# Performance work log

Measured on AMD Instinct MI355X. Metric: run time of the kernel, lower is better.

The kernel has to match this reference:

```python
import jax, jax.numpy as jnp
import numpy as np

N, K, F, E = 1024, 32, 8192, 64   # nodes, max degree, input feats, embed dim
H1, H2 = 128, 64                  # fc MLP widths (layers=[128,64])
T = 3                             # fixed traversal steps per node (original: data-dependent while)


def setup_inputs() -> dict:
    key = jax.random.key(0)
    ks = jax.random.split(key, 8)
    return {
        "feature_origin": jax.random.normal(ks[0], (N, F), jnp.float32),
        "neighbors": jax.random.randint(ks[1], (N, K), 0, N),
        "W_emb": jax.random.normal(ks[2], (F, E), jnp.float32) / np.float32(np.sqrt(F)),
        "b_emb": jnp.zeros((E,), jnp.float32),
        "W1": jax.random.normal(ks[3], (2 * E, H1), jnp.float32) / np.float32(np.sqrt(2 * E)),
        "b1": jnp.zeros((H1,), jnp.float32),
        "W2": jax.random.normal(ks[4], (H1, H2), jnp.float32) / np.float32(np.sqrt(H1)),
        "b2": jnp.zeros((H2,), jnp.float32),
        "W_lk": jax.random.normal(ks[5], (H2, 1), jnp.float32) / np.float32(np.sqrt(H2)),
        "b_lk": jnp.zeros((1,), jnp.float32),
        "W_act": jax.random.normal(ks[6], (H2, 2), jnp.float32) / np.float32(np.sqrt(H2)),
        "b_act": jnp.zeros((2,), jnp.float32),
    }


def reference(feature_origin, neighbors, W_emb, b_emb, W1, b1, W2, b2, W_lk, b_lk, W_act, b_act):
    embed = lambda x: jax.nn.relu(x @ W_emb + b_emb)
    feat0 = embed(feature_origin)  # [N, E]

    def node_step(feature, i):
        idx = neighbors[i]                      # [K] neighbor node ids
        own_orig = feature_origin[i]            # [F]
        valid0 = jnp.ones((K,), bool)
        sum0 = jnp.zeros((F,), feature.dtype)   # running sum of signal-neighbor raw feats
        cnt0 = jnp.zeros((), feature.dtype)
        done0 = jnp.zeros((), bool)

        def step(carry, _):
            feature, valid, sum_hv, cnt, done = carry
            # candidate features: feature[v] if v > 0 else ending zeros (faithful to `v > 0` check)
            cand = jnp.where((idx > 0)[:, None], feature[idx], 0.0)              # [K, E]
            cand = jnp.concatenate([cand, jnp.zeros((1, E), feature.dtype)], 0)  # ending slot -> [K+1, E]
            fi = feature[i]
            s = jnp.concatenate([jnp.broadcast_to(fi, (K + 1, E)), cand], -1)    # [K+1, 2E]
            hidden = jax.nn.relu(jax.nn.relu(s @ W1 + b1) @ W2 + b2)             # [K+1, H2]
            lk = (hidden @ W_lk + b_lk)[:, 0]                                    # [K+1]
            mask = jnp.concatenate([valid, jnp.ones((1,), bool)])                # ending always selectable
            ut = jnp.argmax(jnp.where(mask, lk, -jnp.inf))                       # greedy (in lieu of Categorical)
            new_done = done | (ut == K)
            ut_c = jnp.minimum(ut, K - 1)
            at = jnp.argmax(hidden[ut_c] @ W_act + b_act)                        # greedy action
            u = idx[ut_c]
            u_orig = feature_origin[u]
            take = (at == 1).astype(feature.dtype)
            # hv = mean([signal feats] (+ origin[u] if at==1) + origin[i])
            hv_mean = (sum_hv + take * u_orig + own_orig) / (cnt + take + 1.0)
            new_fi = embed(hv_mean)
            new_fu = embed(u_orig)
            upd = jnp.logical_not(new_done)
            feature = feature.at[i].set(jnp.where(upd, new_fi, feature[i]))
            feature = feature.at[u].set(jnp.where(upd, new_fu, feature[u]))
            sum_hv = jnp.where(upd, sum_hv + take * u_orig, sum_hv)
            cnt = jnp.where(upd, cnt + take, cnt)
            valid = valid.at[ut_c].set(jnp.where(upd, False, valid[ut_c]))  # pop chosen neighbor
            return (feature, valid, sum_hv, cnt, new_done), None

        (feature, _, _, _, _), _ = jax.lax.scan(step, (feature, valid0, sum0, cnt0, done0), None, length=T)
        return feature, None

    feature, _ = jax.lax.scan(jax.checkpoint(node_step), feat0, jnp.arange(N))
    return feature
```

## Files before the change

kernel.cpp:

```cpp
#include <hip/hip_runtime.h>


typedef float f32x4 __attribute__((ext_vector_type(4)));
typedef float f32x2 __attribute__((ext_vector_type(2)));
typedef short bf16x8 __attribute__((ext_vector_type(8)));

__device__ __forceinline__ unsigned short bf16_rne(float x) {
  unsigned u = __builtin_bit_cast(unsigned, x);
  unsigned r = (u + 0x7FFFu + ((u >> 16) & 1u)) >> 16;
  return (unsigned short)r;
}
__device__ __forceinline__ float bf16_f(unsigned short h) {
  return __builtin_bit_cast(float, ((unsigned)h) << 16);
}
__device__ __forceinline__ void split3(float x, unsigned short& h, unsigned short& m,
                                       unsigned short& l) {
  h = bf16_rne(x); float r  = x - bf16_f(h);
  m = bf16_rne(r); float r2 = r - bf16_f(m);
  l = bf16_rne(r2);
}
__device__ __forceinline__ void split3_pk(float x, float y,
                                          unsigned& ph, unsigned& pm, unsigned& pl) {
  asm("v_cvt_pk_bf16_f32 %0, %1, %2" : "=v"(ph) : "v"(x), "v"(y));
  float xh = __builtin_bit_cast(float, ph << 16);
  float yh = __builtin_bit_cast(float, ph & 0xFFFF0000u);
  float rx = x - xh, ry = y - yh;
  asm("v_cvt_pk_bf16_f32 %0, %1, %2" : "=v"(pm) : "v"(rx), "v"(ry));
  float xm = __builtin_bit_cast(float, pm << 16);
  float ym = __builtin_bit_cast(float, pm & 0xFFFF0000u);
  float r2x = rx - xm, r2y = ry - ym;
  asm("v_cvt_pk_bf16_f32 %0, %1, %2" : "=v"(pl) : "v"(r2x), "v"(r2y));
}

__device__ __forceinline__ void bar_lgkm() {
  __builtin_amdgcn_sched_barrier(0);
  asm volatile("s_waitcnt lgkmcnt(0)" ::: "memory");
  __builtin_amdgcn_s_barrier();
  asm volatile("" ::: "memory");
  __builtin_amdgcn_sched_barrier(0);
}

__global__ __launch_bounds__(256) void k_embed(
    const float* __restrict__ X, const float* __restrict__ W_emb,
    const float* __restrict__ b_emb,
    float* __restrict__ G0, float* __restrict__ feat0, float* __restrict__ out)
{
  const int t = threadIdx.x;
  const int j = t & 63;
  const int node = (blockIdx.x << 2) + (t >> 6);
  const float* __restrict__ xr = X + (size_t)node * 8192;
  const float* __restrict__ wp = W_emb + j;
  double a0 = 0.0, a1 = 0.0, a2 = 0.0, a3 = 0.0;
  for (int f = 0; f < 8192; f += 4) {
    float x0 = xr[f + 0], x1 = xr[f + 1], x2 = xr[f + 2], x3 = xr[f + 3];
    a0 = fma((double)x0, (double)wp[(f + 0) << 6], a0);
    a1 = fma((double)x1, (double)wp[(f + 1) << 6], a1);
    a2 = fma((double)x2, (double)wp[(f + 2) << 6], a2);
    a3 = fma((double)x3, (double)wp[(f + 3) << 6], a3);
  }
  float g = (float)((a0 + a1) + (a2 + a3));
  const int o = node * 64 + j;
  G0[o] = g;
  float f0 = fmaxf(g + b_emb[j], 0.0f);
  feat0[o] = f0;
  out[o] = f0;
}

__global__ __launch_bounds__(128) void k_y0(
    const float* __restrict__ feat0, const float* __restrict__ W1,
    float* __restrict__ Y0, float* __restrict__ Y)
{
  const int c = threadIdx.x;
  const int i = blockIdx.x;
  const float* __restrict__ fr = feat0 + i * 64;
  float acc = 0.0f;
  #pragma unroll 8
  for (int e = 0; e < 64; ++e)
    acc = fmaf(fr[e], W1[(64 + e) * 128 + c], acc);
  Y0[i * 128 + c] = acc;
  Y[i * 128 + c] = acc;
}

__global__ __launch_bounds__(512, 2) void k_serial(
    const int* __restrict__ neighbors,
    const float* __restrict__ W1, const float* __restrict__ b1,
    const float* __restrict__ W2, const float* __restrict__ b2,
    const float* __restrict__ W_lk, const float* __restrict__ b_lk,
    const float* __restrict__ W_act, const float* __restrict__ b_act,
    const float* __restrict__ b_emb,
    const float* __restrict__ G0, const float* __restrict__ feat0,
    const float* __restrict__ Y0, float* __restrict__ Y,
    float* __restrict__ feature)
{
  __shared__ __align__(16) float W1T[128 * 130];
  __shared__ __align__(16) unsigned short Ash[48 * 128];
  __shared__ __align__(16) unsigned short Asm[48 * 128];
  __shared__ __align__(16) unsigned short Asl[48 * 128];
  __shared__ __align__(16) float Yl[32][128];
  __shared__ __align__(16) float G0l[32][64];
  __shared__ __align__(16) float a1s[128];
  __shared__ __align__(16) float fis[64];
  __shared__ __align__(16) float b1s[128];
  __shared__ __align__(16) float lkrawT[16][64];
  __shared__ __align__(16) f32x2 p01rawT[16][32];
  __shared__ __align__(16) unsigned keybuf[64];
  __shared__ int idxs[32];
  __shared__ int s_u, s_upd;
  __shared__ unsigned s_mu, s_mi;

  const int t = threadIdx.x;
  const int lane = t & 63;
  const int wave = t >> 6;
  const int l15 = lane & 15;
  const int lg = lane >> 4;
  const int mt = wave & 3;
  const int m0 = mt << 4;
  const int c16 = (mt << 2) + lg;

  unsigned* const uAsh = (unsigned*)Ash;
  unsigned* const uAsm = (unsigned*)Asm;
  unsigned* const uAsl = (unsigned*)Asl;

  for (int idx = t; idx < 16384; idx += 512) {
    int e = idx >> 7, c = idx & 127;
    W1T[c * 130 + e] = W1[e * 128 + c];
  }
  if (t < 128) b1s[t] = b1[t];
  for (int idx = 33 * 64 + t; idx < 48 * 64; idx += 512) {
    uAsh[idx] = 0u; uAsm[idx] = 0u; uAsl[idx] = 0u;
  }
  const float blkv = b_lk[0];
  const float ba0 = b_act[0];
  const float ba1 = b_act[1];
  const float bembr = b_emb[lane];
  bf16x8 wh[4], wm[4], wl[4];
  #pragma unroll
  for (int kc = 0; kc < 4; ++kc) {
    bf16x8 vh, vm, vl;
    #pragma unroll
    for (int e = 0; e < 8; ++e) {
      int k = (kc << 5) + (lg << 3) + e;
      float x = W2[k * 64 + m0 + l15];
      unsigned short sh, sm, sl;
      split3(x, sh, sm, sl);
      vh[e] = (short)sh; vm[e] = (short)sm; vl[e] = (short)sl;
    }
    wh[kc] = vh; wm[kc] = vm; wl[kc] = vl;
  }
  const f32x4 c0init = *(const f32x4*)&b2[m0 + (lg << 2)];
  const f32x4 wl4 = *(const f32x4*)&W_lk[m0 + (lg << 2)];
  f32x4 wa0v, wa1v;
  #pragma unroll
  for (int r = 0; r < 4; ++r) {
    f32x2 w2a = *(const f32x2*)&W_act[(m0 + (lg << 2) + r) << 1];
    wa0v[r] = w2a[0]; wa1v[r] = w2a[1];
  }
  int kk[4]; unsigned wb[4]; const float2* ylp[4];
  #pragma unroll
  for (int n = 0; n < 4; ++n) {
    kk[n] = wave + (n << 3);
    wb[n] = (unsigned)((kk[n] << 6) + (lane ^ ((kk[n] & 7) << 2)));
    ylp[n] = (const float2*)&Yl[kk[n]][lane << 1];
  }
  const unsigned wb32 = 2048u + (unsigned)lane;
  const int ntA = (wave < 4) ? 0 : 1;
  const int rowA = (ntA << 4) + l15;
  const int rowB = 32 + l15;
  int aoA[4], aoB[4];
  #pragma unroll
  for (int kc = 0; kc < 4; ++kc) {
    aoA[kc] = (rowA << 7) + ((((kc << 2) + lg) ^ (rowA & 7)) << 3);
    aoB[kc] = (rowB << 7) + ((((kc << 2) + lg) ^ (rowB & 7)) << 3);
  }
  const float2* const a1p = (const float2*)&a1s[lane << 1];
  unsigned vm = 0xFFFFFFFFu; float cntf = 0.f; int done = 0;
  int ridx = 0; float gisr = 0.f, sumgr = 0.f;

  for (int i = 0; i < 1024; ++i) {
    __syncthreads();
    #pragma unroll
    for (int p = 0; p < 2; ++p) {
      int fi = (p << 9) + t;
      int k = fi >> 5;
      int c4 = (fi & 31) << 2;
      int v = neighbors[(i << 5) + k];
      *(float4*)&Yl[k][c4] = *(const float4*)&Y[v * 128 + c4];
    }
    {
      int k = t >> 4;
      int c4 = (t & 15) << 2;
      int v = neighbors[(i << 5) + k];
      *(float4*)&G0l[k][c4] = *(const float4*)&G0[v * 64 + c4];
    }
    if (t < 64) fis[t] = feature[(i << 6) + t];
    if (t < 32) idxs[t] = neighbors[(i << 5) + t];
    bar_lgkm();
    if (t < 128) {
      float aa0 = b1s[t], aa1 = 0.0f;
      const float* w1r = &W1T[t * 130];
      #pragma unroll 8
      for (int e = 0; e < 64; e += 2) {
        f32x2 wv = *(const f32x2*)&w1r[e];
        aa0 = fmaf(fis[e],     wv[0], aa0);
        aa1 = fmaf(fis[e + 1], wv[1], aa1);
      }
      a1s[t] = aa0 + aa1;
    }
    int vn[4];
    #pragma unroll
    for (int n = 0; n < 4; ++n) vn[n] = idxs[kk[n]];
    if (wave == 0) {
      ridx = idxs[lane & 31];
      gisr = G0[(i << 6) + lane];
      sumgr = 0.f; vm = 0xFFFFFFFFu; cntf = 0.f; done = 0;
    }
    bar_lgkm();

    for (int st = 0; st < 3; ++st) {
      {
        float2 av = *a1p;
        #pragma unroll
        for (int n = 0; n < 4; ++n) {
          float hx = av.x, hy = av.y;
          if (vn[n] > 0) {
            float2 yv = *ylp[n];
            hx += yv.x; hy += yv.y;
          }
          hx = fmaxf(hx, 0.f); hy = fmaxf(hy, 0.f);
          unsigned ph, pm, pl;
          split3_pk(hx, hy, ph, pm, pl);
          uAsh[wb[n]] = ph; uAsm[wb[n]] = pm; uAsl[wb[n]] = pl;
        }
        if (wave == 4) {
          float hx = fmaxf(av.x, 0.f), hy = fmaxf(av.y, 0.f);
          unsigned ph, pm, pl;
          split3_pk(hx, hy, ph, pm, pl);
          uAsh[wb32] = ph; uAsm[wb32] = pm; uAsl[wb32] = pl;
        }
      }
      bar_lgkm();
      {
        f32x4 cA = c0init, cB = c0init;
        const bool twoT = (wave < 4);
        #pragma unroll
        for (int kc = 0; kc < 4; ++kc) {
          bf16x8 ahA = *(const bf16x8*)&Ash[aoA[kc]];
          bf16x8 amA = *(const bf16x8*)&Asm[aoA[kc]];
          bf16x8 alA = *(const bf16x8*)&Asl[aoA[kc]];
          cA = __builtin_amdgcn_mfma_f32_16x16x32_bf16(wh[kc], ahA, cA, 0, 0, 0);
          cA = __builtin_amdgcn_mfma_f32_16x16x32_bf16(wh[kc], amA, cA, 0, 0, 0);
          cA = __builtin_amdgcn_mfma_f32_16x16x32_bf16(wm[kc], ahA, cA, 0, 0, 0);
          cA = __builtin_amdgcn_mfma_f32_16x16x32_bf16(wh[kc], alA, cA, 0, 0, 0);
          cA = __builtin_amdgcn_mfma_f32_16x16x32_bf16(wl[kc], ahA, cA, 0, 0, 0);
          cA = __builtin_amdgcn_mfma_f32_16x16x32_bf16(wm[kc], amA, cA, 0, 0, 0);
          if (twoT) {
            bf16x8 ahB = *(const bf16x8*)&Ash[aoB[kc]];
            bf16x8 amB = *(const bf16x8*)&Asm[aoB[kc]];
            bf16x8 alB = *(const bf16x8*)&Asl[aoB[kc]];
            cB = __builtin_amdgcn_mfma_f32_16x16x32_bf16(wh[kc], ahB, cB, 0, 0, 0);
            cB = __builtin_amdgcn_mfma_f32_16x16x32_bf16(wh[kc], amB, cB, 0, 0, 0);
            cB = __builtin_amdgcn_mfma_f32_16x16x32_bf16(wm[kc], ahB, cB, 0, 0, 0);
            cB = __builtin_amdgcn_mfma_f32_16x16x32_bf16(wh[kc], alB, cB, 0, 0, 0);
            cB = __builtin_amdgcn_mfma_f32_16x16x32_bf16(wl[kc], ahB, cB, 0, 0, 0);
            cB = __builtin_amdgcn_mfma_f32_16x16x32_bf16(wm[kc], amB, cB, 0, 0, 0);
          }
        }
        {
          float pl = 0.f, q0 = 0.f, q1 = 0.f;
          #pragma unroll
          for (int r = 0; r < 4; ++r) {
            float v = fmaxf(cA[r], 0.f);
            pl = fmaf(v, wl4[r], pl);
            q0 = fmaf(v, wa0v[r], q0);
            q1 = fmaf(v, wa1v[r], q1);
          }
          lkrawT[c16][rowA] = pl;
          p01rawT[c16][rowA] = (f32x2){q0, q1};
        }
        if (twoT) {
          float pl = 0.f;
          #pragma unroll
          for (int r = 0; r < 4; ++r) {
            float v = fmaxf(cB[r], 0.f);
            pl = fmaf(v, wl4[r], pl);
          }
          lkrawT[c16][rowB] = pl;
        }
      }
      bar_lgkm();
      if (wave == 0) {
        float v_[16];
        #pragma unroll
        for (int c = 0; c < 16; ++c) v_[c] = lkrawT[c][lane];
        float s0 = (v_[0] + v_[1]) + (v_[2] + v_[3]);
        float s1 = (v_[4] + v_[5]) + (v_[6] + v_[7]);
        float s2 = (v_[8] + v_[9]) + (v_[10] + v_[11]);
        float s3 = (v_[12] + v_[13]) + (v_[14] + v_[15]);
        float lkv = ((s0 + s1) + (s2 + s3)) + blkv;
        unsigned b = __builtin_bit_cast(unsigned, lkv);
        int sb = (int)b >> 31;
        unsigned mono = b ^ (0x80000000u | (unsigned)sb);
        bool valid = (lane == 32) || ((lane < 32) && ((vm >> lane) & 1u));
        unsigned key = valid ? mono : 0u;
        keybuf[lane] = key;
        asm volatile("s_waitcnt lgkmcnt(0)" ::: "memory");
        __builtin_amdgcn_sched_barrier(0);
        const uint4* kb = (const uint4*)keybuf;
        unsigned mx = 0u;
        #pragma unroll
        for (int c = 0; c < 16; ++c) {
          uint4 kv = kb[c];
          unsigned m01 = kv.x > kv.y ? kv.x : kv.y;
          unsigned m23 = kv.z > kv.w ? kv.z : kv.w;
          unsigned mm = m01 > m23 ? m01 : m23;
          mx = mx > mm ? mx : mm;
        }
        unsigned long long am = __ballot(valid && (key == mx));
        const int ut = (int)(__ffsll(am) - 1);
        const int utc = ut < 31 ? ut : 31;
        f32x2 q[16];
        #pragma unroll
        for (int c = 0; c < 16; ++c) q[c] = p01rawT[c][utc];
        f32x2 S0 = (q[0] + q[1]) + (q[2] + q[3]);
        f32x2 S1 = (q[4] + q[5]) + (q[6] + q[7]);
        f32x2 S2 = (q[8] + q[9]) + (q[10] + q[11]);
        f32x2 S3 = (q[12] + q[13]) + (q[14] + q[15]);
        f32x2 D01 = (S0 + S1) + (S2 + S3);
        float d0 = D01[0] + ba0;
        float d1 = D01[1] + ba1;
        const int at1 = (d1 > d0) ? 1 : 0;
        const int newdone = done | (ut == 32);
        const int upd = newdone ? 0 : 1;
        done = newdone;
        const float take = at1 ? 1.0f : 0.0f;
        const float denom = cntf + take + 1.0f;
        const int u = __builtin_amdgcn_readlane(ridx, utc);
        unsigned long long bu = __ballot(lane < 32 && ridx == u);
        unsigned long long bi = __ballot(lane < 32 && ridx == i);
        if (lane == 0) {
          s_u = u; s_upd = upd;
          s_mu = (unsigned)bu; s_mi = (unsigned)bi;
        }
        if (upd) {
          vm &= ~(1u << utc);
          cntf += take;
          const float gu = G0l[utc][lane];
          const float ns = sumgr + take * gu;
          const float hv = (ns + gisr) / denom;
          const float nfi = fmaxf(hv + bembr, 0.0f);
          sumgr = ns;
          const float f0u = fmaxf(gu + bembr, 0.0f);
          feature[(i << 6) + lane] = nfi;
          feature[(u << 6) + lane] = f0u;
          fis[lane] = (u == i) ? f0u : nfi;
        }
      }
      bar_lgkm();
      if (!s_upd) break;
      if (wave < 4) {
        const int u = s_u;
        const int c = t & 127;
        const float* w1r = &W1T[c * 130];
        if (wave < 2) {
          const float yu = Y0[u * 128 + c];
          f32x2 acc = {0.f, 0.f};
          #pragma unroll 8
          for (int e = 0; e < 64; e += 2) {
            f32x2 fv = *(const f32x2*)&fis[e];
            f32x2 wv = *(const f32x2*)&w1r[64 + e];
            acc = __builtin_elementwise_fma(fv, wv, acc);
          }
          const float yi = acc[0] + acc[1];
          Y[i * 128 + c] = yi;
          Y[u * 128 + c] = yu;
          const unsigned mu = s_mu;
          for (unsigned m = mu; m; m &= m - 1) {
            int k = __ffs(m) - 1;
            Yl[k][c] = yu;
          }
          for (unsigned m = s_mi & ~mu; m; m &= m - 1) {
            int k = __ffs(m) - 1;
            Yl[k][c] = yi;
          }
        } else {
          f32x2 aa = {b1s[c], 0.f};
          #pragma unroll 8
          for (int e = 0; e < 64; e += 2) {
            f32x2 fv = *(const f32x2*)&fis[e];
            f32x2 wv = *(const f32x2*)&w1r[e];
            aa = __builtin_elementwise_fma(fv, wv, aa);
          }
          a1s[c] = aa[0] + aa[1];
        }
      }
      bar_lgkm();
    }
  }
}

extern "C" void kernel_launch(void* const* d_in, const int* in_sizes, int n_in,
                              void* d_out, int out_size, void* d_ws, size_t ws_size,
                              hipStream_t stream) {
  const float* X     = (const float*)d_in[0];
  const int*   nbr   = (const int*)  d_in[1];
  const float* W_emb = (const float*)d_in[2];
  const float* b_emb = (const float*)d_in[3];
  const float* W1    = (const float*)d_in[4];
  const float* b1    = (const float*)d_in[5];
  const float* W2    = (const float*)d_in[6];
  const float* b2    = (const float*)d_in[7];
  const float* W_lk  = (const float*)d_in[8];
  const float* b_lk  = (const float*)d_in[9];
  const float* W_act = (const float*)d_in[10];
  const float* b_act = (const float*)d_in[11];
  float* out = (float*)d_out;
  float* ws  = (float*)d_ws;
  float* G0    = ws;
  float* feat0 = ws + 65536;
  float* Y0    = ws + 131072;
  float* Y     = ws + 262144;

  hipLaunchKernelGGL(k_embed, dim3(256), dim3(256), 0, stream,
                     X, W_emb, b_emb, G0, feat0, out);
  hipLaunchKernelGGL(k_y0, dim3(1024), dim3(128), 0, stream,
                     feat0, W1, Y0, Y);
  hipLaunchKernelGGL(k_serial, dim3(1), dim3(512), 0, stream,
                     nbr, W1, b1, W2, b2, W_lk, b_lk, W_act, b_act, b_emb,
                     G0, feat0, Y0, Y, out);
}
```

Measured before the change: 9.194 ms.

## Prefetch next node's neighbor indices and stage Y0 rows in shared memory

Neighbor indices and the node's own G0 row for the next iteration are loaded into registers during the current iteration, which takes the dependent global index load off the critical path of the gather. Y0 rows for all 32 neighbors are also staged in LDS at iteration start, so the per-step Y0[u] read in the serial update comes from shared memory instead of global memory. The cost is more shared memory (another 16KB), which may reduce occupancy, and extra gather traffic each iteration.

```diff
diff --git a/kernel.cpp b/kernel.cpp
--- a/kernel.cpp
+++ b/kernel.cpp
@@ -97,6 +97,7 @@
   __shared__ __align__(16) unsigned short Asm[48 * 128];
   __shared__ __align__(16) unsigned short Asl[48 * 128];
   __shared__ __align__(16) float Yl[32][128];
+  __shared__ __align__(16) float Y0l[32][128];
   __shared__ __align__(16) float G0l[32][64];
   __shared__ __align__(16) float a1s[128];
   __shared__ __align__(16) float fis[64];
@@ -105,7 +106,7 @@
   __shared__ __align__(16) f32x2 p01rawT[16][32];
   __shared__ __align__(16) unsigned keybuf[64];
   __shared__ int idxs[32];
-  __shared__ int s_u, s_upd;
+  __shared__ int s_u, s_upd, s_utc;
   __shared__ unsigned s_mu, s_mi;
 
   const int t = threadIdx.x;
@@ -136,16 +137,16 @@
   bf16x8 wh[4], wm[4], wl[4];
   #pragma unroll
   for (int kc = 0; kc < 4; ++kc) {
-    bf16x8 vh, vm, vl;
+    bf16x8 vh, vm_, vl;
     #pragma unroll
     for (int e = 0; e < 8; ++e) {
       int k = (kc << 5) + (lg << 3) + e;
       float x = W2[k * 64 + m0 + l15];
       unsigned short sh, sm, sl;
       split3(x, sh, sm, sl);
-      vh[e] = (short)sh; vm[e] = (short)sm; vl[e] = (short)sl;
-    }
-    wh[kc] = vh; wm[kc] = vm; wl[kc] = vl;
+      vh[e] = (short)sh; vm_[e] = (short)sm; vl[e] = (short)sl;
+    }
+    wh[kc] = vh; wm[kc] = vm_; wl[kc] = vl;
   }
   const f32x4 c0init = *(const f32x4*)&b2[m0 + (lg << 2)];
   const f32x4 wl4 = *(const f32x4*)&W_lk[m0 + (lg << 2)];
@@ -175,25 +176,38 @@
   const float2* const a1p = (const float2*)&a1s[lane << 1];
   unsigned vm = 0xFFFFFFFFu; float cntf = 0.f; int done = 0;
   int ridx = 0; float gisr = 0.f, sumgr = 0.f;
+  int vA0 = neighbors[t >> 5];
+  int vA1 = neighbors[16 + (t >> 5)];
+  int vB  = neighbors[t >> 4];
+  int vI  = (t < 32) ? neighbors[t] : 0;
+  float gn = (wave == 0) ? G0[lane] : 0.f;
 
   for (int i = 0; i < 1024; ++i) {
     __syncthreads();
-    #pragma unroll
-    for (int p = 0; p < 2; ++p) {
-      int fi = (p << 9) + t;
-      int k = fi >> 5;
-      int c4 = (fi & 31) << 2;
-      int v = neighbors[(i << 5) + k];
-      *(float4*)&Yl[k][c4] = *(const float4*)&Y[v * 128 + c4];
+    const float gcur = gn;
+    {
+      const int c4 = (t & 31) << 2;
+      *(float4*)&Yl [t >> 5][c4]        = *(const float4*)&Y [vA0 * 128 + c4];
+      *(float4*)&Y0l[t >> 5][c4]        = *(const float4*)&Y0[vA0 * 128 + c4];
+      *(float4*)&Yl [16 + (t >> 5)][c4] = *(const float4*)&Y [vA1 * 128 + c4];
+      *(float4*)&Y0l[16 + (t >> 5)][c4] = *(const float4*)&Y0[vA1 * 128 + c4];
     }
     {
       int k = t >> 4;
       int c4 = (t & 15) << 2;
-      int v = neighbors[(i << 5) + k];
-      *(float4*)&G0l[k][c4] = *(const float4*)&G0[v * 64 + c4];
+      *(float4*)&G0l[k][c4] = *(const float4*)&G0[vB * 64 + c4];
     }
     if (t < 64) fis[t] = feature[(i << 6) + t];
-    if (t < 32) idxs[t] = neighbors[(i << 5) + t];
+    if (t < 32) idxs[t] = vI;
+    {
+      int j = (i + 1) & 1023;
+      const int* __restrict__ nb = neighbors + (j << 5);
+      vA0 = nb[t >> 5];
+      vA1 = nb[16 + (t >> 5)];
+      vB  = nb[t >> 4];
+      if (t < 32) vI = nb[t];
+      if (wave == 0) gn = G0[(j << 6) + lane];
+    }
     bar_lgkm();
     if (t < 128) {
       float aa0 = b1s[t], aa1 = 0.0f;
@@ -211,7 +225,7 @@
     for (int n = 0; n < 4; ++n) vn[n] = idxs[kk[n]];
     if (wave == 0) {
       ridx = idxs[lane & 31];
-      gisr = G0[(i << 6) + lane];
+      gisr = gcur;
       sumgr = 0.f; vm = 0xFFFFFFFFu; cntf = 0.f; done = 0;
     }
     bar_lgkm();
@@ -338,7 +352,7 @@
         unsigned long long bu = __ballot(lane < 32 && ridx == u);
         unsigned long long bi = __ballot(lane < 32 && ridx == i);
         if (lane == 0) {
-          s_u = u; s_upd = upd;
+          s_u = u; s_upd = upd; s_utc = utc;
           s_mu = (unsigned)bu; s_mi = (unsigned)bi;
         }
         if (upd) {
@@ -362,7 +376,7 @@
         const int c = t & 127;
         const float* w1r = &W1T[c * 130];
         if (wave < 2) {
-          const float yu = Y0[u * 128 + c];
+          const float yu = Y0l[s_utc][c];
           f32x2 acc = {0.f, 0.f};
           #pragma unroll 8
           for (int e = 0; e < 64; e += 2) {
```

Result: faster. 8.966 ms, median of 2 (-2.5%).
